# Performance work log

Hardware: AMD Instinct MI355X
Metric: run time of the kernel (lower is better)

Reference implementation:

```python
import jax, jax.numpy as jnp
import numpy as np

HEADS = 8
NEG_SLOPE = 0.2  # PyG GATConv default LeakyReLU slope


def _gat_layer(x, src, dst, W, a_src, a_dst, bias, heads, out_ch):
    """PyG-style GATConv (concat heads, self-loops already appended, eval mode).
    x: [N, F_in]; src/dst: [E_tot] int; W: [F_in, heads*out_ch];
    a_src/a_dst: [heads, out_ch]; bias: [heads*out_ch].
    """
    N = x.shape[0]
    h = (x @ W).reshape(N, heads, out_ch)                      # [N, H, C]
    # per-node attention logits (gathered per edge as scalars, not features)
    al_s = jnp.einsum('nhc,hc->nh', h, a_src)                  # [N, H]
    al_d = jnp.einsum('nhc,hc->nh', h, a_dst)                  # [N, H]
    e = jax.nn.leaky_relu(al_s[src] + al_d[dst], negative_slope=NEG_SLOPE)  # [E, H]
    # segment softmax over incoming edges of each target node (stable)
    e_max = jax.ops.segment_max(e, dst, num_segments=N)        # self-loops => no empty segments
    ex = jnp.exp(e - e_max[dst])
    denom = jax.ops.segment_sum(ex, dst, num_segments=N)
    alpha = ex / (denom[dst] + 1e-16)                          # [E, H]
    # gather source features, weight, scatter-add to targets
    out = jax.ops.segment_sum(h[src] * alpha[:, :, None], dst, num_segments=N)  # [N, H, C]
    return out.reshape(N, heads * out_ch) + bias


def setup_inputs() -> dict:
    key = jax.random.key(0)
    ks = jax.random.split(key, 16)
    N, E, F_IN, NUM_CLASSES = 50000, 1600000, 128, 16
    s = 0.1
    return {
        'x': jax.random.normal(ks[0], (N, F_IN), dtype=jnp.float32),
        'edge_index': jax.random.randint(ks[1], (2, E), 0, N, dtype=jnp.int64),
        # GAT layer 1: 128 -> 8 heads x 8
        'W1': jax.random.normal(ks[2], (F_IN, 64), dtype=jnp.float32) * s,
        'a1_src': jax.random.normal(ks[3], (8, 8), dtype=jnp.float32) * s,
        'a1_dst': jax.random.normal(ks[4], (8, 8), dtype=jnp.float32) * s,
        'b1': jnp.zeros((64,), dtype=jnp.float32),
        # GAT layer 2: 64 -> 8 heads x 4
        'W2': jax.random.normal(ks[5], (64, 32), dtype=jnp.float32) * s,
        'a2_src': jax.random.normal(ks[6], (8, 4), dtype=jnp.float32) * s,
        'a2_dst': jax.random.normal(ks[7], (8, 4), dtype=jnp.float32) * s,
        'b2': jnp.zeros((32,), dtype=jnp.float32),
        # torch MultiheadAttention(32, 8): packed in_proj [96,32], out_proj [32,32]
        'in_proj_w': jax.random.normal(ks[8], (96, 32), dtype=jnp.float32) * s,
        'in_proj_b': jnp.zeros((96,), dtype=jnp.float32),
        'out_proj_w': jax.random.normal(ks[9], (32, 32), dtype=jnp.float32) * s,
        'out_proj_b': jnp.zeros((32,), dtype=jnp.float32),
        # fc: 32 -> num_classes
        'fc_w': jax.random.normal(ks[10], (NUM_CLASSES, 32), dtype=jnp.float32) * s,
        'fc_b': jnp.zeros((NUM_CLASSES,), dtype=jnp.float32),
    }


def reference(x, edge_index, W1, a1_src, a1_dst, b1, W2, a2_src, a2_dst, b2,
              in_proj_w, in_proj_b, out_proj_w, out_proj_b, fc_w, fc_b):
    N = x.shape[0]
    loops = jnp.arange(N, dtype=edge_index.dtype)
    src = jnp.concatenate([edge_index[0], loops])  # PyG add_self_loops=True
    dst = jnp.concatenate([edge_index[1], loops])

    h = jax.nn.elu(_gat_layer(x, src, dst, W1, a1_src, a1_dst, b1, HEADS, 8))   # [N, 64]
    h = jax.nn.elu(_gat_layer(h, src, dst, W2, a2_src, a2_dst, b2, HEADS, 4))   # [N, 32]

    # MultiheadAttention on h.unsqueeze(0): shape [1, N, 32] with torch's
    # seq-first layout => seq_len = 1, batch = N. Softmax over a single key
    # is identically 1 for every head, so out = out_proj(v_proj(h)).
    v = h @ in_proj_w[64:96].T + in_proj_b[64:96]   # v-projection slice of packed in_proj
    h = v @ out_proj_w.T + out_proj_b               # [N, 32]

    logits = h @ fc_w.T + fc_b                      # [N, num_classes]
    return jax.nn.log_softmax(logits, axis=1)
```

## Files before the change

### kernel.cpp

```cpp
#include <hip/hip_runtime.h>
#include <hip/hip_bf16.h>
#include <math.h>


#define BSHIFT 7
#define BMASK  ((1 << BSHIFT) - 1)
#define MAXNB  512
#define TILE   8192
#define XST    136
#define SMBYTES 36864
#define LESRC_MAX 6144

typedef __attribute__((ext_vector_type(8))) short short8;
typedef __attribute__((ext_vector_type(4))) float floatx4;
typedef __attribute__((ext_vector_type(2))) float floatx2;

__device__ __forceinline__ unsigned short f2bf(float f) {
    union { float f; unsigned int u; } v; v.f = f;
    unsigned int u = v.u;
    return (unsigned short)((u + 0x7FFFu + ((u >> 16) & 1u)) >> 16);
}
__device__ __forceinline__ float lrelu(float e) { return fmaxf(e, 0.2f * e); }
__device__ __forceinline__ float elu(float o) {
    return (o > 0.f) ? o : (__expf(o) - 1.f);
}

__global__ __launch_bounds__(256) void fused_pre_kernel(
    const float* __restrict__ x, const float* __restrict__ W,
    const float* __restrict__ a_src, const float* __restrict__ a_dst,
    char* __restrict__ rec1, float* __restrict__ ald, int N, int GB,
    const int* __restrict__ ei, int E, int Et, int NB, int CAP,
    int* __restrict__ gcount, unsigned int* __restrict__ rec, int NT,
    const float* __restrict__ in_proj_w, const float* __restrict__ in_proj_b,
    const float* __restrict__ out_proj_w, const float* __restrict__ out_proj_b,
    const float* __restrict__ fc_w, const float* __restrict__ fc_b,
    float* __restrict__ M, float* __restrict__ bf) {
    __shared__ __align__(16) char sm[SMBYTES];
    int t = threadIdx.x;
    int bid = blockIdx.x;
    if (bid < GB) {
        unsigned short* xs = (unsigned short*)sm;
        unsigned short* wt = xs + 64 * XST;
        int nb = bid * 64;
// ... 2 lines not shown
            int p = t + 256 * r;
            int row = p >> 5;
            int c4  = p & 31;
            int n = nb + row;
            float4 v = (n < N) ? ((const float4*)x)[(size_t)n * 32 + c4]
                               : make_float4(0.f, 0.f, 0.f, 0.f);
            unsigned short* dst = &xs[row * XST + c4 * 4];
            dst[0] = f2bf(v.x); dst[1] = f2bf(v.y);
            dst[2] = f2bf(v.z); dst[3] = f2bf(v.w);
        }
        {
            int n = t & 63, kg = t >> 6;
#pragma unroll
            for (int c = 0; c < 4; ++c) {
                int k0 = kg * 32 + c * 8;
                unsigned short* dst = &wt[n * XST + k0];
#pragma unroll
                for (int j = 0; j < 8; ++j)
                    dst[j] = f2bf(W[(k0 + j) * 64 + n]);
            }
        }
        __syncthreads();
        int wave = t >> 6, lane = t & 63;
        int m16 = lane & 15, quad = lane >> 4;
        floatx4 acc[4];
#pragma unroll
        for (int i = 0; i < 4; ++i) acc[i] = (floatx4){0.f, 0.f, 0.f, 0.f};
#pragma unroll
        for (int k = 0; k < 4; ++k) {
            int koff = k * 32 + quad * 8;
            short8 afrag = *(const short8*)&xs[(wave * 16 + m16) * XST + koff];
#pragma unroll
            for (int nt = 0; nt < 4; ++nt) {
                short8 bfrag = *(const short8*)&wt[(nt * 16 + m16) * XST + koff];
// ... 5 lines not shown
#pragma unroll
        for (int nt = 0; nt < 4; ++nt)
#pragma unroll
            for (int r = 0; r < 4; ++r)
                hs[(wave * 16 + quad * 4 + r) * 65 + nt * 16 + m16] = acc[nt][r];
        __syncthreads();
        float asv = a_src[lane], adv = a_dst[lane];
        for (int itn = 0; itn < 16; ++itn) {
            int nl = wave * 16 + itn;
            int n = nb + nl;
            if (n >= N) break;
            float v = hs[nl * 65 + lane];
            float ps = v * asv, pd = v * adv;
            ps += __shfl_xor(ps, 1); ps += __shfl_xor(ps, 2); ps += __shfl_xor(ps, 4);
            pd += __shfl_xor(pd, 1); pd += __shfl_xor(pd, 2); pd += __shfl_xor(pd, 4);
            if ((lane & 7) == 0) {
                *(float*)(rec1 + (size_t)n * 128 + 4 * (lane >> 3)) = ps;
                ald[n * 8 + (lane >> 3)] = pd;
            }
            if (lane < 16) {
                const float* hr = &hs[nl * 65 + lane * 4];
                int pk = __builtin_amdgcn_cvt_pk_fp8_f32(hr[0], hr[1], 0, false);
                pk = __builtin_amdgcn_cvt_pk_fp8_f32(hr[2], hr[3], pk, true);
                *(unsigned*)(rec1 + (size_t)n * 128 + 64 + 4 * lane) = (unsigned)pk;
            }
        }
    } else if (bid < GB + NT) {
        unsigned int* lrec = (unsigned int*)sm;
        int* h   = (int*)(sm + TILE * 4);
        int* cur = (int*)(sm + TILE * 4 + MAXNB * 4);
        for (int i = t; i < NB; i += 256) h[i] = 0;
        int tile0 = (bid - GB) * TILE;
        int cnt = Et - tile0; if (cnt > TILE) cnt = TILE;
        __syncthreads();
        for (int j = t; j < cnt; j += 256) {
            int jj = tile0 + j;
            int srcv, d;
            if (jj < E) { srcv = ei[jj]; d = ei[E + jj]; } else { srcv = jj - E; d = jj - E; }
            lrec[j] = (unsigned)srcv | ((unsigned)d << 16);
// ... 89 lines not shown
    for (int i = t; i < cnt; i += 256)
        esrc[obase + i] = lesrc[i];
}

__global__ __launch_bounds__(256) void gat_agg64_g2_kernel(
    const int* __restrict__ rowp, const unsigned short* __restrict__ esrc,
    const char* __restrict__ rec1, const float* __restrict__ ald_arr,
    const float* __restrict__ bias,
    const float* __restrict__ W2, const float* __restrict__ a2s,
    const float* __restrict__ a2d,
    char* __restrict__ rec2, float* __restrict__ ald2, int N) {
    __shared__ __align__(16) float W2p[2][8][32][4];
    __shared__ __align__(16) float oL[4][64];
    __shared__ __align__(16) float h2L[4][32];
    int t = threadIdx.x;
    for (int idx = t; idx < 2048; idx += 256) {
        int k = idx >> 5, l = idx & 31;
        W2p[k >> 5][(k & 31) >> 2][l][k & 3] = W2[idx];
    }
    __syncthreads();
    const int lane = t & 63;
    const int wv = t >> 6;
    const int e = lane >> 3;
    const int c = lane & 7;
    const int aoff = 4 * c;
    const int foff = 64 + 8 * c;
    int n = blockIdx.x * 4 + wv;
    if (n >= N) return;
    float aldv = ald_arr[n * 8 + c];
    int beg = rowp[n], end = rowp[n + 1];
    float dA = 0.f, dB = 0.f;
    floatx2 A0 = {0.f, 0.f}, A1 = {0.f, 0.f}, A2 = {0.f, 0.f}, A3 = {0.f, 0.f};
    floatx2 B0 = {0.f, 0.f}, B1 = {0.f, 0.f}, B2 = {0.f, 0.f}, B3 = {0.f, 0.f};
    int i = beg;
    for (; i + 32 <= end; i += 32) {
        int s0 = esrc[i + e],      s1 = esrc[i + 8 + e];
        int s2 = esrc[i + 16 + e], s3 = esrc[i + 24 + e];
        const char* r0 = rec1 + (size_t)s0 * 128;
        const char* r1 = rec1 + (size_t)s1 * 128;
        const char* r2 = rec1 + (size_t)s2 * 128;
        const char* r3 = rec1 + (size_t)s3 * 128;
        float e0 = *(const float*)(r0 + aoff), e1 = *(const float*)(r1 + aoff);
        float e2 = *(const float*)(r2 + aoff), e3 = *(const float*)(r3 + aoff);
        uint2 g0 = *(const uint2*)(r0 + foff), g1 = *(const uint2*)(r1 + foff);
        uint2 g2 = *(const uint2*)(r2 + foff), g3 = *(const uint2*)(r3 + foff);
        float w0 = __expf(lrelu(e0 + aldv));
        float w1 = __expf(lrelu(e1 + aldv));
        float w2 = __expf(lrelu(e2 + aldv));
        float w3 = __expf(lrelu(e3 + aldv));
        dA += w0 + w2; dB += w1 + w3;
        A0 += w0 * __builtin_amdgcn_cvt_pk_f32_fp8(g0.x, false);
        A1 += w0 * __builtin_amdgcn_cvt_pk_f32_fp8(g0.x, true);
        A2 += w0 * __builtin_amdgcn_cvt_pk_f32_fp8(g0.y, false);
        A3 += w0 * __builtin_amdgcn_cvt_pk_f32_fp8(g0.y, true);
        B0 += w1 * __builtin_amdgcn_cvt_pk_f32_fp8(g1.x, false);
        B1 += w1 * __builtin_amdgcn_cvt_pk_f32_fp8(g1.x, true);
        B2 += w1 * __builtin_amdgcn_cvt_pk_f32_fp8(g1.y, false);
        B3 += w1 * __builtin_amdgcn_cvt_pk_f32_fp8(g1.y, true);
        A0 += w2 * __builtin_amdgcn_cvt_pk_f32_fp8(g2.x, false);
        A1 += w2 * __builtin_amdgcn_cvt_pk_f32_fp8(g2.x, true);
        A2 += w2 * __builtin_amdgcn_cvt_pk_f32_fp8(g2.y, false);
        A3 += w2 * __builtin_amdgcn_cvt_pk_f32_fp8(g2.y, true);
        B0 += w3 * __builtin_amdgcn_cvt_pk_f32_fp8(g3.x, false);
        B1 += w3 * __builtin_amdgcn_cvt_pk_f32_fp8(g3.x, true);
        B2 += w3 * __builtin_amdgcn_cvt_pk_f32_fp8(g3.y, false);
        B3 += w3 * __builtin_amdgcn_cvt_pk_f32_fp8(g3.y, true);
    }
    for (; i < end; i += 32) {
        int i0 = i + e, i1 = i + 8 + e, i2 = i + 16 + e, i3 = i + 24 + e;
        bool v0 = i0 < end, v1 = i1 < end, v2 = i2 < end, v3 = i3 < end;
        int c0 = v0 ? i0 : beg;
        int c1 = v1 ? i1 : beg;
        int c2 = v2 ? i2 : beg;
        int c3 = v3 ? i3 : beg;
        int s0 = esrc[c0], s1 = esrc[c1], s2 = esrc[c2], s3 = esrc[c3];
        const char* r0 = rec1 + (size_t)s0 * 128;
        const char* r1 = rec1 + (size_t)s1 * 128;
        const char* r2 = rec1 + (size_t)s2 * 128;
        const char* r3 = rec1 + (size_t)s3 * 128;
        float e0 = *(const float*)(r0 + aoff), e1 = *(const float*)(r1 + aoff);
        float e2 = *(const float*)(r2 + aoff), e3 = *(const float*)(r3 + aoff);
        uint2 g0 = *(const uint2*)(r0 + foff), g1 = *(const uint2*)(r1 + foff);
        uint2 g2 = *(const uint2*)(r2 + foff), g3 = *(const uint2*)(r3 + foff);
        float w0 = v0 ? __expf(lrelu(e0 + aldv)) : 0.f;
        float w1 = v1 ? __expf(lrelu(e1 + aldv)) : 0.f;
        float w2 = v2 ? __expf(lrelu(e2 + aldv)) : 0.f;
        float w3 = v3 ? __expf(lrelu(e3 + aldv)) : 0.f;
        dA += w0 + w2; dB += w1 + w3;
        A0 += w0 * __builtin_amdgcn_cvt_pk_f32_fp8(g0.x, false);
        A1 += w0 * __builtin_amdgcn_cvt_pk_f32_fp8(g0.x, true);
        A2 += w0 * __builtin_amdgcn_cvt_pk_f32_fp8(g0.y, false);
        A3 += w0 * __builtin_amdgcn_cvt_pk_f32_fp8(g0.y, true);
        B0 += w1 * __builtin_amdgcn_cvt_pk_f32_fp8(g1.x, false);
        B1 += w1 * __builtin_amdgcn_cvt_pk_f32_fp8(g1.x, true);
        B2 += w1 * __builtin_amdgcn_cvt_pk_f32_fp8(g1.y, false);
        B3 += w1 * __builtin_amdgcn_cvt_pk_f32_fp8(g1.y, true);
        A0 += w2 * __builtin_amdgcn_cvt_pk_f32_fp8(g2.x, false);
        A1 += w2 * __builtin_amdgcn_cvt_pk_f32_fp8(g2.x, true);
        A2 += w2 * __builtin_amdgcn_cvt_pk_f32_fp8(g2.y, false);
        A3 += w2 * __builtin_amdgcn_cvt_pk_f32_fp8(g2.y, true);
        B0 += w3 * __builtin_amdgcn_cvt_pk_f32_fp8(g3.x, false);
        B1 += w3 * __builtin_amdgcn_cvt_pk_f32_fp8(g3.x, true);
        B2 += w3 * __builtin_amdgcn_cvt_pk_f32_fp8(g3.y, false);
        B3 += w3 * __builtin_amdgcn_cvt_pk_f32_fp8(g3.y, true);
    }
    float d = dA + dB;
    float P0 = A0.x + B0.x, P1 = A0.y + B0.y;
    float P2 = A1.x + B1.x, P3 = A1.y + B1.y;
    float P4 = A2.x + B2.x, P5 = A2.y + B2.y;
    float P6 = A3.x + B3.x, P7 = A3.y + B3.y;
    d  += __shfl_xor(d, 8);  d  += __shfl_xor(d, 16);  d  += __shfl_xor(d, 32);
    P0 += __shfl_xor(P0, 8); P0 += __shfl_xor(P0, 16); P0 += __shfl_xor(P0, 32);
    P1 += __shfl_xor(P1, 8); P1 += __shfl_xor(P1, 16); P1 += __shfl_xor(P1, 32);
    P2 += __shfl_xor(P2, 8); P2 += __shfl_xor(P2, 16); P2 += __shfl_xor(P2, 32);
    P3 += __shfl_xor(P3, 8); P3 += __shfl_xor(P3, 16); P3 += __shfl_xor(P3, 32);
    P4 += __shfl_xor(P4, 8); P4 += __shfl_xor(P4, 16); P4 += __shfl_xor(P4, 32);
    P5 += __shfl_xor(P5, 8); P5 += __shfl_xor(P5, 16); P5 += __shfl_xor(P5, 32);
    P6 += __shfl_xor(P6, 8); P6 += __shfl_xor(P6, 16); P6 += __shfl_xor(P6, 32);
    P7 += __shfl_xor(P7, 8); P7 += __shfl_xor(P7, 16); P7 += __shfl_xor(P7, 32);
    float inv = 1.f / (d + 1e-16f);
    float4 bv0 = ((const float4*)bias)[2 * c];
    float4 bv1 = ((const float4*)bias)[2 * c + 1];
    float o0 = elu(P0 * inv + bv0.x);
    float o1 = elu(P1 * inv + bv0.y);
    float o2 = elu(P2 * inv + bv0.z);
    float o3 = elu(P3 * inv + bv0.w);
    float o4 = elu(P4 * inv + bv1.x);
    float o5 = elu(P5 * inv + bv1.y);
    float o6 = elu(P6 * inv + bv1.z);
    float o7 = elu(P7 * inv + bv1.w);
    if (lane < 8) {
        *(float4*)&oL[wv][c * 8]     = make_float4(o0, o1, o2, o3);
        *(float4*)&oL[wv][c * 8 + 4] = make_float4(o4, o5, o6, o7);
    }
    const int l = lane & 31, kh = lane >> 5;
    const float* orow = &oL[wv][kh * 32];
    float a0 = 0.f, a1 = 0.f, a2 = 0.f, a3 = 0.f;
#pragma unroll
    for (int g = 0; g < 8; ++g) {
        float4 ov = *(const float4*)&orow[g * 4];
        float4 wv4 = *(const float4*)&W2p[kh][g][l][0];
        a0 += ov.x * wv4.x; a1 += ov.y * wv4.y;
        a2 += ov.z * wv4.z; a3 += ov.w * wv4.w;
    }
    float acc = (a0 + a1) + (a2 + a3);
    acc += __shfl_xor(acc, 32);
    float ps = acc * a2s[l], pd = acc * a2d[l];
    ps += __shfl_xor(ps, 1); ps += __shfl_xor(ps, 2);
    pd += __shfl_xor(pd, 1); pd += __shfl_xor(pd, 2);
    if (lane < 32) {
        h2L[wv][l] = acc;
        if ((l & 3) == 0) {
            *(float*)(rec2 + (size_t)n * 64 + 4 * (l >> 2)) = ps;
            ald2[n * 8 + (l >> 2)] = pd;
        }
    }
    if (lane < 8) {
        const float* hr = &h2L[wv][lane * 4];
        int pk = __builtin_amdgcn_cvt_pk_fp8_f32(hr[0], hr[1], 0, false);
        pk = __builtin_amdgcn_cvt_pk_fp8_f32(hr[2], hr[3], pk, true);
        *(unsigned*)(rec2 + (size_t)n * 64 + 32 + 4 * lane) = (unsigned)pk;
    }
}

__global__ __launch_bounds__(256) void gat_agg32_fin_kernel(
    const int* __restrict__ rowp, const unsigned short* __restrict__ esrc,
    const char* __restrict__ rec2, const float* __restrict__ ald_arr,
    const float* __restrict__ bias,
    const float* __restrict__ M, const float* __restrict__ bf,
    float* __restrict__ out, int N) {
    __shared__ __align__(16) float Mp[8][16][4];
    __shared__ float bfs[16];
    __shared__ __align__(16) float oL[4][32];
    int t = threadIdx.x;
    for (int i = t; i < 512; i += 256) {
        int j = i >> 5, k = i & 31;
        Mp[k >> 2][j][k & 3] = M[i];
    }
    if (t < 16) bfs[t] = bf[t];
    __syncthreads();
    const int lane = t & 63;
    const int wv = t >> 6;
    const int e = lane >> 3;
    const int c = lane & 7;
    const int aoff = 4 * c;
    const int foff = 32 + 4 * c;
    int n = blockIdx.x * 4 + wv;
    if (n >= N) return;
    float aldv = ald_arr[n * 8 + c];
    int beg = rowp[n], end = rowp[n + 1];
    float d0 = 0.f, d1 = 0.f, d2 = 0.f, d3 = 0.f;
    floatx2 p0a = {0.f, 0.f}, p0b = {0.f, 0.f};
    floatx2 p1a = {0.f, 0.f}, p1b = {0.f, 0.f};
    floatx2 p2a = {0.f, 0.f}, p2b = {0.f, 0.f};
    floatx2 p3a = {0.f, 0.f}, p3b = {0.f, 0.f};
    int base = beg;
    for (; base + 32 <= end; base += 32) {
        int s0 = esrc[base + e],      s1 = esrc[base + 8 + e];
        int s2 = esrc[base + 16 + e], s3 = esrc[base + 24 + e];
        const char* r0 = rec2 + (size_t)s0 * 64;
        const char* r1 = rec2 + (size_t)s1 * 64;
        const char* r2 = rec2 + (size_t)s2 * 64;
        const char* r3 = rec2 + (size_t)s3 * 64;
        float e0 = *(const float*)(r0 + aoff) + aldv;
        float e1 = *(const float*)(r1 + aoff) + aldv;
        float e2 = *(const float*)(r2 + aoff) + aldv;
        float e3 = *(const float*)(r3 + aoff) + aldv;
        unsigned g0 = *(const unsigned*)(r0 + foff);
        unsigned g1 = *(const unsigned*)(r1 + foff);
        unsigned g2 = *(const unsigned*)(r2 + foff);
        unsigned g3 = *(const unsigned*)(r3 + foff);
        float w0 = __expf(lrelu(e0));
        float w1 = __expf(lrelu(e1));
        float w2 = __expf(lrelu(e2));
        float w3 = __expf(lrelu(e3));
        d0 += w0; d1 += w1; d2 += w2; d3 += w3;
        p0a += w0 * __builtin_amdgcn_cvt_pk_f32_fp8(g0, false);
        p0b += w0 * __builtin_amdgcn_cvt_pk_f32_fp8(g0, true);
        p1a += w1 * __builtin_amdgcn_cvt_pk_f32_fp8(g1, false);
        p1b += w1 * __builtin_amdgcn_cvt_pk_f32_fp8(g1, true);
        p2a += w2 * __builtin_amdgcn_cvt_pk_f32_fp8(g2, false);
        p2b += w2 * __builtin_amdgcn_cvt_pk_f32_fp8(g2, true);
        p3a += w3 * __builtin_amdgcn_cvt_pk_f32_fp8(g3, false);
        p3b += w3 * __builtin_amdgcn_cvt_pk_f32_fp8(g3, true);
    }
    for (; base < end; base += 32) {
        int i0 = base + e;
        int i1 = base + 8 + e;
        int i2 = base + 16 + e;
        int i3 = base + 24 + e;
        bool v0 = i0 < end, v1 = i1 < end, v2 = i2 < end, v3 = i3 < end;
        int c0 = v0 ? i0 : beg;
        int c1 = v1 ? i1 : beg;
        int c2 = v2 ? i2 : beg;
        int c3 = v3 ? i3 : beg;
        int s0 = esrc[c0], s1 = esrc[c1], s2 = esrc[c2], s3 = esrc[c3];
        const char* r0 = rec2 + (size_t)s0 * 64;
        const char* r1 = rec2 + (size_t)s1 * 64;
        const char* r2 = rec2 + (size_t)s2 * 64;
        const char* r3 = rec2 + (size_t)s3 * 64;
        float e0 = *(const float*)(r0 + aoff) + aldv;
        float e1 = *(const float*)(r1 + aoff) + aldv;
        float e2 = *(const float*)(r2 + aoff) + aldv;
        float e3 = *(const float*)(r3 + aoff) + aldv;
        unsigned g0 = *(const unsigned*)(r0 + foff);
        unsigned g1 = *(const unsigned*)(r1 + foff);
        unsigned g2 = *(const unsigned*)(r2 + foff);
        unsigned g3 = *(const unsigned*)(r3 + foff);
        float w0 = v0 ? __expf(lrelu(e0)) : 0.f;
        float w1 = v1 ? __expf(lrelu(e1)) : 0.f;
        float w2 = v2 ? __expf(lrelu(e2)) : 0.f;
        float w3 = v3 ? __expf(lrelu(e3)) : 0.f;
        d0 += w0; d1 += w1; d2 += w2; d3 += w3;
        p0a += w0 * __builtin_amdgcn_cvt_pk_f32_fp8(g0, false);
        p0b += w0 * __builtin_amdgcn_cvt_pk_f32_fp8(g0, true);
        p1a += w1 * __builtin_amdgcn_cvt_pk_f32_fp8(g1, false);
        p1b += w1 * __builtin_amdgcn_cvt_pk_f32_fp8(g1, true);
        p2a += w2 * __builtin_amdgcn_cvt_pk_f32_fp8(g2, false);
        p2b += w2 * __builtin_amdgcn_cvt_pk_f32_fp8(g2, true);
        p3a += w3 * __builtin_amdgcn_cvt_pk_f32_fp8(g3, false);
        p3b += w3 * __builtin_amdgcn_cvt_pk_f32_fp8(g3, true);
    }
    float d = (d0 + d1) + (d2 + d3);
    floatx2 Pa = (p0a + p1a) + (p2a + p3a);
    floatx2 Pb = (p0b + p1b) + (p2b + p3b);
    float P0 = Pa.x, P1 = Pa.y, P2 = Pb.x, P3 = Pb.y;
    d  += __shfl_xor(d, 8);  d  += __shfl_xor(d, 16);  d  += __shfl_xor(d, 32);
    P0 += __shfl_xor(P0, 8); P0 += __shfl_xor(P0, 16); P0 += __shfl_xor(P0, 32);
    P1 += __shfl_xor(P1, 8); P1 += __shfl_xor(P1, 16); P1 += __shfl_xor(P1, 32);
    P2 += __shfl_xor(P2, 8); P2 += __shfl_xor(P2, 16); P2 += __shfl_xor(P2, 32);
    P3 += __shfl_xor(P3, 8); P3 += __shfl_xor(P3, 16); P3 += __shfl_xor(P3, 32);
    float inv = 1.f / (d + 1e-16f);
    float4 bv = ((const float4*)bias)[c];
    float o0 = elu(P0 * inv + bv.x);
    float o1 = elu(P1 * inv + bv.y);
    float o2 = elu(P2 * inv + bv.z);
    float o3 = elu(P3 * inv + bv.w);
    if (lane < 8) *(float4*)&oL[wv][c * 4] = make_float4(o0, o1, o2, o3);
    const int j = lane & 15;
    const float* orow = oL[wv];
    float a0 = 0.f, a1 = 0.f, a2 = 0.f, a3 = 0.f;
#pragma unroll
    for (int g = 0; g < 8; ++g) {
        float4 ov = *(const float4*)&orow[g * 4];
        float4 mv = *(const float4*)&Mp[g][j][0];
        a0 += ov.x * mv.x; a1 += ov.y * mv.y;
        a2 += ov.z * mv.z; a3 += ov.w * mv.w;
    }
    float logit = (a0 + a1) + (a2 + a3) + bfs[j];
    float mx = logit;
    mx = fmaxf(mx, __shfl_xor(mx, 1));
    mx = fmaxf(mx, __shfl_xor(mx, 2));
    mx = fmaxf(mx, __shfl_xor(mx, 4));
// ... 46 lines not shown
        void* p = ws + off;
        off += bytes;
        off = (off + 255) & ~(size_t)255;
        return p;
    };
    int*   bcount = (int*)alloc(MAXNB * 4);
    unsigned int*   rec  = (unsigned int*)alloc((size_t)NB * CAP * 4);
    int*   rowp   = (int*)alloc((size_t)(N + 1) * 4);
    unsigned short* esrc = (unsigned short*)alloc((size_t)Et * 2);
    char* rec1   = (char*)alloc((size_t)N * 128);
    float* al1d  = (float*)alloc((size_t)N * 8 * 4);
    char* rec2   = (char*)alloc((size_t)N * 64);
    float* al2d  = (float*)alloc((size_t)N * 8 * 4);
    float* Mf    = (float*)alloc(512 * 4);
    float* bff   = (float*)alloc(16 * 4);
    (void)ws_size; (void)n_in; (void)out_size;

    hipMemsetAsync(bcount, 0, MAXNB * 4, stream);
    fused_pre_kernel<<<GB + NTILES + 1, 256, 0, stream>>>(
        x, W1, a1s, a1d, rec1, al1d, N, GB,
        ei, E, Et, NB, CAP, bcount, rec, NTILES,
        ipw, ipb, opw, opb, fcw, fcb, Mf, bff);
    csr_finalize_kernel<<<NB, 256, 0, stream>>>(rec, bcount, rowp, esrc, N, Et, CAP);

    gat_agg64_g2_kernel<<<(N + 3) / 4, 256, 0, stream>>>(
        rowp, esrc, rec1, al1d, b1, W2, a2s, a2d, rec2, al2d, N);
    gat_agg32_fin_kernel<<<(N + 3) / 4, 256, 0, stream>>>(
        rowp, esrc, rec2, al2d, b2, Mf, bff, out, N);
}
```

Baseline: 212.3 us.

## Interleave per-head logits with fp8 features and fully unroll low-degree gathers

The layer-1 node record is changed so each head stores its attention logit next to its 8 fp8 features in one 16-byte chunk. The aggregation kernel can then fetch both with a single uint4 load per edge instead of separate float and uint2 loads. Both aggregation kernels add a fast path for nodes with degree up to 48 or 64 that issues all gathers up front, which gives more memory-level parallelism. The W2/M shared-memory staging moves after the gather so it overlaps with the loads. A small prep kernel also pre-converts W1 to bf16 and replaces the memset, at the cost of an extra launch and padded record bytes.

```diff
diff --git a/kernel.cpp b/kernel.cpp
--- a/kernel.cpp
+++ b/kernel.cpp
@@ -25,8 +25,18 @@
     return (o > 0.f) ? o : (__expf(o) - 1.f);
 }
 
+__global__ __launch_bounds__(256) void prep_kernel(
+    const float* __restrict__ W, unsigned short* __restrict__ wtb,
+    int* __restrict__ gcount) {
+    int t = threadIdx.x;
+    if (blockIdx.x == 0) { gcount[t] = 0; gcount[t + 256] = 0; }
+    int idx = blockIdx.x * 256 + t;
+    int n = idx >> 7, k = idx & 127;
+    wtb[idx] = f2bf(W[k * 64 + n]);
+}
+
 __global__ __launch_bounds__(256) void fused_pre_kernel(
-    const float* __restrict__ x, const float* __restrict__ W,
+    const float* __restrict__ x, const unsigned short* __restrict__ wtb,
     const float* __restrict__ a_src, const float* __restrict__ a_dst,
     char* __restrict__ rec1, float* __restrict__ ald, int N, int GB,
     const int* __restrict__ ei, int E, int Et, int NB, int CAP,
@@ -59,10 +69,7 @@
 #pragma unroll
             for (int c = 0; c < 4; ++c) {
                 int k0 = kg * 32 + c * 8;
-                unsigned short* dst = &wt[n * XST + k0];
-#pragma unroll
-                for (int j = 0; j < 8; ++j)
-                    dst[j] = f2bf(W[(k0 + j) * 64 + n]);
+                *(short8*)&wt[n * XST + k0] = *(const short8*)&wtb[n * 128 + k0];
             }
         }
         __syncthreads();
@@ -98,15 +105,21 @@
             float ps = v * asv, pd = v * adv;
             ps += __shfl_xor(ps, 1); ps += __shfl_xor(ps, 2); ps += __shfl_xor(ps, 4);
             pd += __shfl_xor(pd, 1); pd += __shfl_xor(pd, 2); pd += __shfl_xor(pd, 4);
-            if ((lane & 7) == 0) {
-                *(float*)(rec1 + (size_t)n * 128 + 4 * (lane >> 3)) = ps;
+            float av = __shfl(ps, (lane & 7) * 8);
+            if ((lane & 7) == 0)
                 ald[n * 8 + (lane >> 3)] = pd;
-            }
-            if (lane < 16) {
-                const float* hr = &hs[nl * 65 + lane * 4];
-                int pk = __builtin_amdgcn_cvt_pk_fp8_f32(hr[0], hr[1], 0, false);
-                pk = __builtin_amdgcn_cvt_pk_fp8_f32(hr[2], hr[3], pk, true);
-                *(unsigned*)(rec1 + (size_t)n * 128 + 64 + 4 * lane) = (unsigned)pk;
+            if (lane < 8) {
+                const float* hr = &hs[nl * 65 + lane * 8];
+                int pk0 = __builtin_amdgcn_cvt_pk_fp8_f32(hr[0], hr[1], 0, false);
+                pk0 = __builtin_amdgcn_cvt_pk_fp8_f32(hr[2], hr[3], pk0, true);
+                int pk1 = __builtin_amdgcn_cvt_pk_fp8_f32(hr[4], hr[5], 0, false);
+                pk1 = __builtin_amdgcn_cvt_pk_fp8_f32(hr[6], hr[7], pk1, true);
+                uint4 w4;
+                w4.x = __float_as_uint(av);
+                w4.y = (unsigned)pk0;
+                w4.z = (unsigned)pk1;
+                w4.w = 0u;
+                *(uint4*)(rec1 + (size_t)n * 128 + lane * 16) = w4;
             }
         }
     } else if (bid < GB + NT) {
@@ -226,125 +239,150 @@
     __shared__ __align__(16) float oL[4][64];
     __shared__ __align__(16) float h2L[4][32];
     int t = threadIdx.x;
-    for (int idx = t; idx < 2048; idx += 256) {
-        int k = idx >> 5, l = idx & 31;
-        W2p[k >> 5][(k & 31) >> 2][l][k & 3] = W2[idx];
-    }
-    __syncthreads();
     const int lane = t & 63;
     const int wv = t >> 6;
     const int e = lane >> 3;
     const int c = lane & 7;
-    const int aoff = 4 * c;
-    const int foff = 64 + 8 * c;
     int n = blockIdx.x * 4 + wv;
-    if (n >= N) return;
-    float aldv = ald_arr[n * 8 + c];
-    int beg = rowp[n], end = rowp[n + 1];
-    float dA = 0.f, dB = 0.f;
-    floatx2 A0 = {0.f, 0.f}, A1 = {0.f, 0.f}, A2 = {0.f, 0.f}, A3 = {0.f, 0.f};
-    floatx2 B0 = {0.f, 0.f}, B1 = {0.f, 0.f}, B2 = {0.f, 0.f}, B3 = {0.f, 0.f};
-    int i = beg;
-    for (; i + 32 <= end; i += 32) {
-        int s0 = esrc[i + e],      s1 = esrc[i + 8 + e];
-        int s2 = esrc[i + 16 + e], s3 = esrc[i + 24 + e];
-        const char* r0 = rec1 + (size_t)s0 * 128;
-        const char* r1 = rec1 + (size_t)s1 * 128;
-        const char* r2 = rec1 + (size_t)s2 * 128;
-        const char* r3 = rec1 + (size_t)s3 * 128;
-        float e0 = *(const float*)(r0 + aoff), e1 = *(const float*)(r1 + aoff);
-        float e2 = *(const float*)(r2 + aoff), e3 = *(const float*)(r3 + aoff);
-        uint2 g0 = *(const uint2*)(r0 + foff), g1 = *(const uint2*)(r1 + foff);
-        uint2 g2 = *(const uint2*)(r2 + foff), g3 = *(const uint2*)(r3 + foff);
-        float w0 = __expf(lrelu(e0 + aldv));
-        float w1 = __expf(lrelu(e1 + aldv));
-        float w2 = __expf(lrelu(e2 + aldv));
-        float w3 = __expf(lrelu(e3 + aldv));
-        dA += w0 + w2; dB += w1 + w3;
-        A0 += w0 * __builtin_amdgcn_cvt_pk_f32_fp8(g0.x, false);
-        A1 += w0 * __builtin_amdgcn_cvt_pk_f32_fp8(g0.x, true);
-        A2 += w0 * __builtin_amdgcn_cvt_pk_f32_fp8(g0.y, false);
-        A3 += w0 * __builtin_amdgcn_cvt_pk_f32_fp8(g0.y, true);
-        B0 += w1 * __builtin_amdgcn_cvt_pk_f32_fp8(g1.x, false);
-        B1 += w1 * __builtin_amdgcn_cvt_pk_f32_fp8(g1.x, true);
-        B2 += w1 * __builtin_amdgcn_cvt_pk_f32_fp8(g1.y, false);
-        B3 += w1 * __builtin_amdgcn_cvt_pk_f32_fp8(g1.y, true);
-        A0 += w2 * __builtin_amdgcn_cvt_pk_f32_fp8(g2.x, false);
-        A1 += w2 * __builtin_amdgcn_cvt_pk_f32_fp8(g2.x, true);
-        A2 += w2 * __builtin_amdgcn_cvt_pk_f32_fp8(g2.y, false);
-        A3 += w2 * __builtin_amdgcn_cvt_pk_f32_fp8(g2.y, true);
-        B0 += w3 * __builtin_amdgcn_cvt_pk_f32_fp8(g3.x, false);
-        B1 += w3 * __builtin_amdgcn_cvt_pk_f32_fp8(g3.x, true);
-        B2 += w3 * __builtin_amdgcn_cvt_pk_f32_fp8(g3.y, false);
-        B3 += w3 * __builtin_amdgcn_cvt_pk_f32_fp8(g3.y, true);
-    }
-    for (; i < end; i += 32) {
-        int i0 = i + e, i1 = i + 8 + e, i2 = i + 16 + e, i3 = i + 24 + e;
-        bool v0 = i0 < end, v1 = i1 < end, v2 = i2 < end, v3 = i3 < end;
-        int c0 = v0 ? i0 : beg;
-        int c1 = v1 ? i1 : beg;
-        int c2 = v2 ? i2 : beg;
-        int c3 = v3 ? i3 : beg;
-        int s0 = esrc[c0], s1 = esrc[c1], s2 = esrc[c2], s3 = esrc[c3];
-        const char* r0 = rec1 + (size_t)s0 * 128;
-        const char* r1 = rec1 + (size_t)s1 * 128;
-        const char* r2 = rec1 + (size_t)s2 * 128;
-        const char* r3 = rec1 + (size_t)s3 * 128;
-        float e0 = *(const float*)(r0 + aoff), e1 = *(const float*)(r1 + aoff);
-        float e2 = *(const float*)(r2 + aoff), e3 = *(const float*)(r3 + aoff);
-        uint2 g0 = *(const uint2*)(r0 + foff), g1 = *(const uint2*)(r1 + foff);
-        uint2 g2 = *(const uint2*)(r2 + foff), g3 = *(const uint2*)(r3 + foff);
-        float w0 = v0 ? __expf(lrelu(e0 + aldv)) : 0.f;
-        float w1 = v1 ? __expf(lrelu(e1 + aldv)) : 0.f;
-        float w2 = v2 ? __expf(lrelu(e2 + aldv)) : 0.f;
-        float w3 = v3 ? __expf(lrelu(e3 + aldv)) : 0.f;
-        dA += w0 + w2; dB += w1 + w3;
-        A0 += w0 * __builtin_amdgcn_cvt_pk_f32_fp8(g0.x, false);
-        A1 += w0 * __builtin_amdgcn_cvt_pk_f32_fp8(g0.x, true);
-        A2 += w0 * __builtin_amdgcn_cvt_pk_f32_fp8(g0.y, false);
-        A3 += w0 * __builtin_amdgcn_cvt_pk_f32_fp8(g0.y, true);
-        B0 += w1 * __builtin_amdgcn_cvt_pk_f32_fp8(g1.x, false);
-        B1 += w1 * __builtin_amdgcn_cvt_pk_f32_fp8(g1.x, true);
-        B2 += w1 * __builtin_amdgcn_cvt_pk_f32_fp8(g1.y, false);
-        B3 += w1 * __builtin_amdgcn_cvt_pk_f32_fp8(g1.y, true);
-        A0 += w2 * __builtin_amdgcn_cvt_pk_f32_fp8(g2.x, false);
-        A1 += w2 * __builtin_amdgcn_cvt_pk_f32_fp8(g2.x, true);
-        A2 += w2 * __builtin_amdgcn_cvt_pk_f32_fp8(g2.y, false);
-        A3 += w2 * __builtin_amdgcn_cvt_pk_f32_fp8(g2.y, true);
-        B0 += w3 * __builtin_amdgcn_cvt_pk_f32_fp8(g3.x, false);
-        B1 += w3 * __builtin_amdgcn_cvt_pk_f32_fp8(g3.x, true);
-        B2 += w3 * __builtin_amdgcn_cvt_pk_f32_fp8(g3.y, false);
-        B3 += w3 * __builtin_amdgcn_cvt_pk_f32_fp8(g3.y, true);
-    }
-    float d = dA + dB;
-    float P0 = A0.x + B0.x, P1 = A0.y + B0.y;
-    float P2 = A1.x + B1.x, P3 = A1.y + B1.y;
-    float P4 = A2.x + B2.x, P5 = A2.y + B2.y;
-    float P6 = A3.x + B3.x, P7 = A3.y + B3.y;
-    d  += __shfl_xor(d, 8);  d  += __shfl_xor(d, 16);  d  += __shfl_xor(d, 32);
-    P0 += __shfl_xor(P0, 8); P0 += __shfl_xor(P0, 16); P0 += __shfl_xor(P0, 32);
-    P1 += __shfl_xor(P1, 8); P1 += __shfl_xor(P1, 16); P1 += __shfl_xor(P1, 32);
-    P2 += __shfl_xor(P2, 8); P2 += __shfl_xor(P2, 16); P2 += __shfl_xor(P2, 32);
-    P3 += __shfl_xor(P3, 8); P3 += __shfl_xor(P3, 16); P3 += __shfl_xor(P3, 32);
-    P4 += __shfl_xor(P4, 8); P4 += __shfl_xor(P4, 16); P4 += __shfl_xor(P4, 32);
-    P5 += __shfl_xor(P5, 8); P5 += __shfl_xor(P5, 16); P5 += __shfl_xor(P5, 32);
-    P6 += __shfl_xor(P6, 8); P6 += __shfl_xor(P6, 16); P6 += __shfl_xor(P6, 32);
-    P7 += __shfl_xor(P7, 8); P7 += __shfl_xor(P7, 16); P7 += __shfl_xor(P7, 32);
-    float inv = 1.f / (d + 1e-16f);
-    float4 bv0 = ((const float4*)bias)[2 * c];
-    float4 bv1 = ((const float4*)bias)[2 * c + 1];
-    float o0 = elu(P0 * inv + bv0.x);
-    float o1 = elu(P1 * inv + bv0.y);
-    float o2 = elu(P2 * inv + bv0.z);
-    float o3 = elu(P3 * inv + bv0.w);
-    float o4 = elu(P4 * inv + bv1.x);
-    float o5 = elu(P5 * inv + bv1.y);
-    float o6 = elu(P6 * inv + bv1.z);
-    float o7 = elu(P7 * inv + bv1.w);
-    if (lane < 8) {
-        *(float4*)&oL[wv][c * 8]     = make_float4(o0, o1, o2, o3);
-        *(float4*)&oL[wv][c * 8 + 4] = make_float4(o4, o5, o6, o7);
-    }
+    bool active = n < N;
+    if (active) {
+        float aldv = ald_arr[n * 8 + c];
+        int beg = rowp[n], end = rowp[n + 1];
+        int deg = end - beg;
+        float dA = 0.f, dB = 0.f;
+        floatx2 A0 = {0.f, 0.f}, A1 = {0.f, 0.f}, A2 = {0.f, 0.f}, A3 = {0.f, 0.f};
+        floatx2 B0 = {0.f, 0.f}, B1 = {0.f, 0.f}, B2 = {0.f, 0.f}, B3 = {0.f, 0.f};
+        if (deg <= 48) {
+            int s[6];
+#pragma unroll
+            for (int g = 0; g < 6; ++g) {
+                int p = beg + g * 8 + e;
+                s[g] = esrc[(p < end) ? p : beg];
+            }
+            uint4 r[6];
+#pragma unroll
+            for (int g = 0; g < 6; ++g)
+                r[g] = *(const uint4*)(rec1 + (size_t)s[g] * 128 + c * 16);
+#pragma unroll
+            for (int g = 0; g < 6; ++g) {
+                bool vv = (beg + g * 8 + e) < end;
+                float w = vv ? __expf(lrelu(__uint_as_float(r[g].x) + aldv)) : 0.f;
+                if ((g & 1) == 0) {
+                    dA += w;
+                    A0 += w * __builtin_amdgcn_cvt_pk_f32_fp8(r[g].y, false);
+                    A1 += w * __builtin_amdgcn_cvt_pk_f32_fp8(r[g].y, true);
+                    A2 += w * __builtin_amdgcn_cvt_pk_f32_fp8(r[g].z, false);
+                    A3 += w * __builtin_amdgcn_cvt_pk_f32_fp8(r[g].z, true);
+                } else {
+                    dB += w;
+                    B0 += w * __builtin_amdgcn_cvt_pk_f32_fp8(r[g].y, false);
+                    B1 += w * __builtin_amdgcn_cvt_pk_f32_fp8(r[g].y, true);
+                    B2 += w * __builtin_amdgcn_cvt_pk_f32_fp8(r[g].z, false);
+                    B3 += w * __builtin_amdgcn_cvt_pk_f32_fp8(r[g].z, true);
+                }
+            }
+        } else {
+            int i = beg;
+            for (; i + 32 <= end; i += 32) {
+                int s0 = esrc[i + e],      s1 = esrc[i + 8 + e];
+                int s2 = esrc[i + 16 + e], s3 = esrc[i + 24 + e];
+                uint4 r0 = *(const uint4*)(rec1 + (size_t)s0 * 128 + c * 16);
+                uint4 r1 = *(const uint4*)(rec1 + (size_t)s1 * 128 + c * 16);
+                uint4 r2 = *(const uint4*)(rec1 + (size_t)s2 * 128 + c * 16);
+                uint4 r3 = *(const uint4*)(rec1 + (size_t)s3 * 128 + c * 16);
+                float w0 = __expf(lrelu(__uint_as_float(r0.x) + aldv));
+                float w1 = __expf(lrelu(__uint_as_float(r1.x) + aldv));
+                float w2 = __expf(lrelu(__uint_as_float(r2.x) + aldv));
+                float w3 = __expf(lrelu(__uint_as_float(r3.x) + aldv));
+                dA += w0 + w2; dB += w1 + w3;
+                A0 += w0 * __builtin_amdgcn_cvt_pk_f32_fp8(r0.y, false);
+                A1 += w0 * __builtin_amdgcn_cvt_pk_f32_fp8(r0.y, true);
+                A2 += w0 * __builtin_amdgcn_cvt_pk_f32_fp8(r0.z, false);
+                A3 += w0 * __builtin_amdgcn_cvt_pk_f32_fp8(r0.z, true);
+                B0 += w1 * __builtin_amdgcn_cvt_pk_f32_fp8(r1.y, false);
+                B1 += w1 * __builtin_amdgcn_cvt_pk_f32_fp8(r1.y, true);
+                B2 += w1 * __builtin_amdgcn_cvt_pk_f32_fp8(r1.z, false);
+                B3 += w1 * __builtin_amdgcn_cvt_pk_f32_fp8(r1.z, true);
+                A0 += w2 * __builtin_amdgcn_cvt_pk_f32_fp8(r2.y, false);
+                A1 += w2 * __builtin_amdgcn_cvt_pk_f32_fp8(r2.y, true);
+                A2 += w2 * __builtin_amdgcn_cvt_pk_f32_fp8(r2.z, false);
+                A3 += w2 * __builtin_amdgcn_cvt_pk_f32_fp8(r2.z, true);
+                B0 += w3 * __builtin_amdgcn_cvt_pk_f32_fp8(r3.y, false);
+                B1 += w3 * __builtin_amdgcn_cvt_pk_f32_fp8(r3.y, true);
+                B2 += w3 * __builtin_amdgcn_cvt_pk_f32_fp8(r3.z, false);
+                B3 += w3 * __builtin_amdgcn_cvt_pk_f32_fp8(r3.z, true);
+            }
+            for (; i < end; i += 32) {
+                int i0 = i + e, i1 = i + 8 + e, i2 = i + 16 + e, i3 = i + 24 + e;
+                bool v0 = i0 < end, v1 = i1 < end, v2 = i2 < end, v3 = i3 < end;
+                int c0 = v0 ? i0 : beg;
+                int c1 = v1 ? i1 : beg;
+                int c2 = v2 ? i2 : beg;
+                int c3 = v3 ? i3 : beg;
+                int s0 = esrc[c0], s1 = esrc[c1], s2 = esrc[c2], s3 = esrc[c3];
+                uint4 r0 = *(const uint4*)(rec1 + (size_t)s0 * 128 + c * 16);
+                uint4 r1 = *(const uint4*)(rec1 + (size_t)s1 * 128 + c * 16);
+                uint4 r2 = *(const uint4*)(rec1 + (size_t)s2 * 128 + c * 16);
+                uint4 r3 = *(const uint4*)(rec1 + (size_t)s3 * 128 + c * 16);
+                float w0 = v0 ? __expf(lrelu(__uint_as_float(r0.x) + aldv)) : 0.f;
+                float w1 = v1 ? __expf(lrelu(__uint_as_float(r1.x) + aldv)) : 0.f;
+                float w2 = v2 ? __expf(lrelu(__uint_as_float(r2.x) + aldv)) : 0.f;
+                float w3 = v3 ? __expf(lrelu(__uint_as_float(r3.x) + aldv)) : 0.f;
+                dA += w0 + w2; dB += w1 + w3;
+                A0 += w0 * __builtin_amdgcn_cvt_pk_f32_fp8(r0.y, false);
+                A1 += w0 * __builtin_amdgcn_cvt_pk_f32_fp8(r0.y, true);
+                A2 += w0 * __builtin_amdgcn_cvt_pk_f32_fp8(r0.z, false);
+                A3 += w0 * __builtin_amdgcn_cvt_pk_f32_fp8(r0.z, true);
+                B0 += w1 * __builtin_amdgcn_cvt_pk_f32_fp8(r1.y, false);
+                B1 += w1 * __builtin_amdgcn_cvt_pk_f32_fp8(r1.y, true);
+                B2 += w1 * __builtin_amdgcn_cvt_pk_f32_fp8(r1.z, false);
+                B3 += w1 * __builtin_amdgcn_cvt_pk_f32_fp8(r1.z, true);
+                A0 += w2 * __builtin_amdgcn_cvt_pk_f32_fp8(r2.y, false);
+                A1 += w2 * __builtin_amdgcn_cvt_pk_f32_fp8(r2.y, true);
+                A2 += w2 * __builtin_amdgcn_cvt_pk_f32_fp8(r2.z, false);
+                A3 += w2 * __builtin_amdgcn_cvt_pk_f32_fp8(r2.z, true);
+                B0 += w3 * __builtin_amdgcn_cvt_pk_f32_fp8(r3.y, false);
+                B1 += w3 * __builtin_amdgcn_cvt_pk_f32_fp8(r3.y, true);
+                B2 += w3 * __builtin_amdgcn_cvt_pk_f32_fp8(r3.z, false);
+                B3 += w3 * __builtin_amdgcn_cvt_pk_f32_fp8(r3.z, true);
+            }
+        }
+        float d = dA + dB;
+        float P0 = A0.x + B0.x, P1 = A0.y + B0.y;
+        float P2 = A1.x + B1.x, P3 = A1.y + B1.y;
+        float P4 = A2.x + B2.x, P5 = A2.y + B2.y;
+        float P6 = A3.x + B3.x, P7 = A3.y + B3.y;
+        d  += __shfl_xor(d, 8);  d  += __shfl_xor(d, 16);  d  += __shfl_xor(d, 32);
+        P0 += __shfl_xor(P0, 8); P0 += __shfl_xor(P0, 16); P0 += __shfl_xor(P0, 32);
+        P1 += __shfl_xor(P1, 8); P1 += __shfl_xor(P1, 16); P1 += __shfl_xor(P1, 32);
+        P2 += __shfl_xor(P2, 8); P2 += __shfl_xor(P2, 16); P2 += __shfl_xor(P2, 32);
+        P3 += __shfl_xor(P3, 8); P3 += __shfl_xor(P3, 16); P3 += __shfl_xor(P3, 32);
+        P4 += __shfl_xor(P4, 8); P4 += __shfl_xor(P4, 16); P4 += __shfl_xor(P4, 32);
+        P5 += __shfl_xor(P5, 8); P5 += __shfl_xor(P5, 16); P5 += __shfl_xor(P5, 32);
+        P6 += __shfl_xor(P6, 8); P6 += __shfl_xor(P6, 16); P6 += __shfl_xor(P6, 32);
+        P7 += __shfl_xor(P7, 8); P7 += __shfl_xor(P7, 16); P7 += __shfl_xor(P7, 32);
+        float inv = 1.f / (d + 1e-16f);
+        float4 bv0 = ((const float4*)bias)[2 * c];
+        float4 bv1 = ((const float4*)bias)[2 * c + 1];
+        float o0 = elu(P0 * inv + bv0.x);
+        float o1 = elu(P1 * inv + bv0.y);
+        float o2 = elu(P2 * inv + bv0.z);
+        float o3 = elu(P3 * inv + bv0.w);
+        float o4 = elu(P4 * inv + bv1.x);
+        float o5 = elu(P5 * inv + bv1.y);
+        float o6 = elu(P6 * inv + bv1.z);
+        float o7 = elu(P7 * inv + bv1.w);
+        if (lane < 8) {
+            *(float4*)&oL[wv][c * 8]     = make_float4(o0, o1, o2, o3);
+            *(float4*)&oL[wv][c * 8 + 4] = make_float4(o4, o5, o6, o7);
+        }
+    }
+    for (int idx = t; idx < 2048; idx += 256) {
+        int k = idx >> 5, l = idx & 31;
+        W2p[k >> 5][(k & 31) >> 2][l][k & 3] = W2[idx];
+    }
+    __syncthreads();
+    if (!active) return;
     const int l = lane & 31, kh = lane >> 5;
     const float* orow = &oL[wv][kh * 32];
     float a0 = 0.f, a1 = 0.f, a2 = 0.f, a3 = 0.f;
@@ -360,18 +398,19 @@
     float ps = acc * a2s[l], pd = acc * a2d[l];
     ps += __shfl_xor(ps, 1); ps += __shfl_xor(ps, 2);
     pd += __shfl_xor(pd, 1); pd += __shfl_xor(pd, 2);
+    float psv = __shfl(ps, (lane & 7) * 4);
     if (lane < 32) {
         h2L[wv][l] = acc;
-        if ((l & 3) == 0) {
-            *(float*)(rec2 + (size_t)n * 64 + 4 * (l >> 2)) = ps;
-            ald2[n * 8 + (l >> 2)] = pd;
-        }
+        if ((l & 3) == 0) ald2[n * 8 + (l >> 2)] = pd;
     }
     if (lane < 8) {
         const float* hr = &h2L[wv][lane * 4];
         int pk = __builtin_amdgcn_cvt_pk_fp8_f32(hr[0], hr[1], 0, false);
         pk = __builtin_amdgcn_cvt_pk_fp8_f32(hr[2], hr[3], pk, true);
-        *(unsigned*)(rec2 + (size_t)n * 64 + 32 + 4 * lane) = (unsigned)pk;
+        uint2 w2;
+        w2.x = __float_as_uint(psv);
+        w2.y = (unsigned)pk;
+        *(uint2*)(rec2 + (size_t)n * 64 + lane * 8) = w2;
     }
 }
 
@@ -385,110 +424,131 @@
     __shared__ float bfs[16];
     __shared__ __align__(16) float oL[4][32];
     int t = threadIdx.x;
-    for (int i = t; i < 512; i += 256) {
-        int j = i >> 5, k = i & 31;
-        Mp[k >> 2][j][k & 3] = M[i];
-    }
-    if (t < 16) bfs[t] = bf[t];
-    __syncthreads();
     const int lane = t & 63;
     const int wv = t >> 6;
     const int e = lane >> 3;
     const int c = lane & 7;
-    const int aoff = 4 * c;
-    const int foff = 32 + 4 * c;
     int n = blockIdx.x * 4 + wv;
-    if (n >= N) return;
-    float aldv = ald_arr[n * 8 + c];
-    int beg = rowp[n], end = rowp[n + 1];
-    float d0 = 0.f, d1 = 0.f, d2 = 0.f, d3 = 0.f;
-    floatx2 p0a = {0.f, 0.f}, p0b = {0.f, 0.f};
-    floatx2 p1a = {0.f, 0.f}, p1b = {0.f, 0.f};
-    floatx2 p2a = {0.f, 0.f}, p2b = {0.f, 0.f};
-    floatx2 p3a = {0.f, 0.f}, p3b = {0.f, 0.f};
-    int base = beg;
-    for (; base + 32 <= end; base += 32) {
-        int s0 = esrc[base + e],      s1 = esrc[base + 8 + e];
-        int s2 = esrc[base + 16 + e], s3 = esrc[base + 24 + e];
-        const char* r0 = rec2 + (size_t)s0 * 64;
-        const char* r1 = rec2 + (size_t)s1 * 64;
-        const char* r2 = rec2 + (size_t)s2 * 64;
-        const char* r3 = rec2 + (size_t)s3 * 64;
-        float e0 = *(const float*)(r0 + aoff) + aldv;
-        float e1 = *(const float*)(r1 + aoff) + aldv;
-        float e2 = *(const float*)(r2 + aoff) + aldv;
-        float e3 = *(const float*)(r3 + aoff) + aldv;
-        unsigned g0 = *(const unsigned*)(r0 + foff);
-        unsigned g1 = *(const unsigned*)(r1 + foff);
-        unsigned g2 = *(const unsigned*)(r2 + foff);
-        unsigned g3 = *(const unsigned*)(r3 + foff);
-        float w0 = __expf(lrelu(e0));
-        float w1 = __expf(lrelu(e1));
-        float w2 = __expf(lrelu(e2));
-        float w3 = __expf(lrelu(e3));
-        d0 += w0; d1 += w1; d2 += w2; d3 += w3;
-        p0a += w0 * __builtin_amdgcn_cvt_pk_f32_fp8(g0, false);
-        p0b += w0 * __builtin_amdgcn_cvt_pk_f32_fp8(g0, true);
-        p1a += w1 * __builtin_amdgcn_cvt_pk_f32_fp8(g1, false);
-        p1b += w1 * __builtin_amdgcn_cvt_pk_f32_fp8(g1, true);
-        p2a += w2 * __builtin_amdgcn_cvt_pk_f32_fp8(g2, false);
-        p2b += w2 * __builtin_amdgcn_cvt_pk_f32_fp8(g2, true);
-        p3a += w3 * __builtin_amdgcn_cvt_pk_f32_fp8(g3, false);
-        p3b += w3 * __builtin_amdgcn_cvt_pk_f32_fp8(g3, true);
-    }
-    for (; base < end; base += 32) {
-        int i0 = base + e;
-        int i1 = base + 8 + e;
-        int i2 = base + 16 + e;
-        int i3 = base + 24 + e;
-        bool v0 = i0 < end, v1 = i1 < end, v2 = i2 < end, v3 = i3 < end;
-        int c0 = v0 ? i0 : beg;
-        int c1 = v1 ? i1 : beg;
-        int c2 = v2 ? i2 : beg;
-        int c3 = v3 ? i3 : beg;
-        int s0 = esrc[c0], s1 = esrc[c1], s2 = esrc[c2], s3 = esrc[c3];
-        const char* r0 = rec2 + (size_t)s0 * 64;
-        const char* r1 = rec2 + (size_t)s1 * 64;
-        const char* r2 = rec2 + (size_t)s2 * 64;
-        const char* r3 = rec2 + (size_t)s3 * 64;
-        float e0 = *(const float*)(r0 + aoff) + aldv;
-        float e1 = *(const float*)(r1 + aoff) + aldv;
-        float e2 = *(const float*)(r2 + aoff) + aldv;
-        float e3 = *(const float*)(r3 + aoff) + aldv;
-        unsigned g0 = *(const unsigned*)(r0 + foff);
-        unsigned g1 = *(const unsigned*)(r1 + foff);
-        unsigned g2 = *(const unsigned*)(r2 + foff);
-        unsigned g3 = *(const unsigned*)(r3 + foff);
-        float w0 = v0 ? __expf(lrelu(e0)) : 0.f;
-        float w1 = v1 ? __expf(lrelu(e1)) : 0.f;
-        float w2 = v2 ? __expf(lrelu(e2)) : 0.f;
-        float w3 = v3 ? __expf(lrelu(e3)) : 0.f;
-        d0 += w0; d1 += w1; d2 += w2; d3 += w3;
-        p0a += w0 * __builtin_amdgcn_cvt_pk_f32_fp8(g0, false);
-        p0b += w0 * __builtin_amdgcn_cvt_pk_f32_fp8(g0, true);
-        p1a += w1 * __builtin_amdgcn_cvt_pk_f32_fp8(g1, false);
-        p1b += w1 * __builtin_amdgcn_cvt_pk_f32_fp8(g1, true);
-        p2a += w2 * __builtin_amdgcn_cvt_pk_f32_fp8(g2, false);
-        p2b += w2 * __builtin_amdgcn_cvt_pk_f32_fp8(g2, true);
-        p3a += w3 * __builtin_amdgcn_cvt_pk_f32_fp8(g3, false);
-        p3b += w3 * __builtin_amdgcn_cvt_pk_f32_fp8(g3, true);
-    }
-    float d = (d0 + d1) + (d2 + d3);
-    floatx2 Pa = (p0a + p1a) + (p2a + p3a);
-    floatx2 Pb = (p0b + p1b) + (p2b + p3b);
-    float P0 = Pa.x, P1 = Pa.y, P2 = Pb.x, P3 = Pb.y;
-    d  += __shfl_xor(d, 8);  d  += __shfl_xor(d, 16);  d  += __shfl_xor(d, 32);
-    P0 += __shfl_xor(P0, 8); P0 += __shfl_xor(P0, 16); P0 += __shfl_xor(P0, 32);
-    P1 += __shfl_xor(P1, 8); P1 += __shfl_xor(P1, 16); P1 += __shfl_xor(P1, 32);
-    P2 += __shfl_xor(P2, 8); P2 += __shfl_xor(P2, 16); P2 += __shfl_xor(P2, 32);
-    P3 += __shfl_xor(P3, 8); P3 += __shfl_xor(P3, 16); P3 += __shfl_xor(P3, 32);
-    float inv = 1.f / (d + 1e-16f);
-    float4 bv = ((const float4*)bias)[c];
-    float o0 = elu(P0 * inv + bv.x);
-    float o1 = elu(P1 * inv + bv.y);
-    float o2 = elu(P2 * inv + bv.z);
-    float o3 = elu(P3 * inv + bv.w);
-    if (lane < 8) *(float4*)&oL[wv][c * 4] = make_float4(o0, o1, o2, o3);
+    bool active = n < N;
+    if (active) {
+        float aldv = ald_arr[n * 8 + c];
+        int beg = rowp[n], end = rowp[n + 1];
+        int deg = end - beg;
+        float d0 = 0.f, d1 = 0.f, d2 = 0.f, d3 = 0.f;
+        floatx2 p0a = {0.f, 0.f}, p0b = {0.f, 0.f};
+        floatx2 p1a = {0.f, 0.f}, p1b = {0.f, 0.f};
+        floatx2 p2a = {0.f, 0.f}, p2b = {0.f, 0.f};
+        floatx2 p3a = {0.f, 0.f}, p3b = {0.f, 0.f};
+        if (deg <= 64) {
+            int s[8];
+#pragma unroll
+            for (int g = 0; g < 8; ++g) {
+                int p = beg + g * 8 + e;
+                s[g] = esrc[(p < end) ? p : beg];
+            }
+            uint2 rr[8];
+#pragma unroll
+            for (int g = 0; g < 8; ++g)
+                rr[g] = *(const uint2*)(rec2 + (size_t)s[g] * 64 + c * 8);
+#pragma unroll
+            for (int g = 0; g < 8; ++g) {
+                bool vv = (beg + g * 8 + e) < end;
+                float w = vv ? __expf(lrelu(__uint_as_float(rr[g].x) + aldv)) : 0.f;
+                if ((g & 3) == 0) {
+                    d0 += w;
+                    p0a += w * __builtin_amdgcn_cvt_pk_f32_fp8(rr[g].y, false);
+                    p0b += w * __builtin_amdgcn_cvt_pk_f32_fp8(rr[g].y, true);
+                } else if ((g & 3) == 1) {
+                    d1 += w;
+                    p1a += w * __builtin_amdgcn_cvt_pk_f32_fp8(rr[g].y, false);
+                    p1b += w * __builtin_amdgcn_cvt_pk_f32_fp8(rr[g].y, true);
+                } else if ((g & 3) == 2) {
+                    d2 += w;
+                    p2a += w * __builtin_amdgcn_cvt_pk_f32_fp8(rr[g].y, false);
+                    p2b += w * __builtin_amdgcn_cvt_pk_f32_fp8(rr[g].y, true);
+                } else {
+                    d3 += w;
+                    p3a += w * __builtin_amdgcn_cvt_pk_f32_fp8(rr[g].y, false);
+                    p3b += w * __builtin_amdgcn_cvt_pk_f32_fp8(rr[g].y, true);
+                }
+            }
+        } else {
+            int base = beg;
+            for (; base + 32 <= end; base += 32) {
+                int s0 = esrc[base + e],      s1 = esrc[base + 8 + e];
+                int s2 = esrc[base + 16 + e], s3 = esrc[base + 24 + e];
+                uint2 r0 = *(const uint2*)(rec2 + (size_t)s0 * 64 + c * 8);
+                uint2 r1 = *(const uint2*)(rec2 + (size_t)s1 * 64 + c * 8);
+                uint2 r2 = *(const uint2*)(rec2 + (size_t)s2 * 64 + c * 8);
+                uint2 r3 = *(const uint2*)(rec2 + (size_t)s3 * 64 + c * 8);
+                float w0 = __expf(lrelu(__uint_as_float(r0.x) + aldv));
+                float w1 = __expf(lrelu(__uint_as_float(r1.x) + aldv));
+                float w2 = __expf(lrelu(__uint_as_float(r2.x) + aldv));
+                float w3 = __expf(lrelu(__uint_as_float(r3.x) + aldv));
+                d0 += w0; d1 += w1; d2 += w2; d3 += w3;
+                p0a += w0 * __builtin_amdgcn_cvt_pk_f32_fp8(r0.y, false);
+                p0b += w0 * __builtin_amdgcn_cvt_pk_f32_fp8(r0.y, true);
+                p1a += w1 * __builtin_amdgcn_cvt_pk_f32_fp8(r1.y, false);
+                p1b += w1 * __builtin_amdgcn_cvt_pk_f32_fp8(r1.y, true);
+                p2a += w2 * __builtin_amdgcn_cvt_pk_f32_fp8(r2.y, false);
+                p2b += w2 * __builtin_amdgcn_cvt_pk_f32_fp8(r2.y, true);
+                p3a += w3 * __builtin_amdgcn_cvt_pk_f32_fp8(r3.y, false);
+                p3b += w3 * __builtin_amdgcn_cvt_pk_f32_fp8(r3.y, true);
+            }
+            for (; base < end; base += 32) {
+                int i0 = base + e;
+                int i1 = base + 8 + e;
+                int i2 = base + 16 + e;
+                int i3 = base + 24 + e;
+                bool v0 = i0 < end, v1 = i1 < end, v2 = i2 < end, v3 = i3 < end;
+                int c0 = v0 ? i0 : beg;
+                int c1 = v1 ? i1 : beg;
+                int c2 = v2 ? i2 : beg;
+                int c3 = v3 ? i3 : beg;
+                int s0 = esrc[c0], s1 = esrc[c1], s2 = esrc[c2], s3 = esrc[c3];
+                uint2 r0 = *(const uint2*)(rec2 + (size_t)s0 * 64 + c * 8);
+                uint2 r1 = *(const uint2*)(rec2 + (size_t)s1 * 64 + c * 8);
+                uint2 r2 = *(const uint2*)(rec2 + (size_t)s2 * 64 + c * 8);
+                uint2 r3 = *(const uint2*)(rec2 + (size_t)s3 * 64 + c * 8);
+                float w0 = v0 ? __expf(lrelu(__uint_as_float(r0.x) + aldv)) : 0.f;
+                float w1 = v1 ? __expf(lrelu(__uint_as_float(r1.x) + aldv)) : 0.f;
+                float w2 = v2 ? __expf(lrelu(__uint_as_float(r2.x) + aldv)) : 0.f;
+                float w3 = v3 ? __expf(lrelu(__uint_as_float(r3.x) + aldv)) : 0.f;
+                d0 += w0; d1 += w1; d2 += w2; d3 += w3;
+                p0a += w0 * __builtin_amdgcn_cvt_pk_f32_fp8(r0.y, false);
+                p0b += w0 * __builtin_amdgcn_cvt_pk_f32_fp8(r0.y, true);
+                p1a += w1 * __builtin_amdgcn_cvt_pk_f32_fp8(r1.y, false);
+                p1b += w1 * __builtin_amdgcn_cvt_pk_f32_fp8(r1.y, true);
+                p2a += w2 * __builtin_amdgcn_cvt_pk_f32_fp8(r2.y, false);
+                p2b += w2 * __builtin_amdgcn_cvt_pk_f32_fp8(r2.y, true);
+                p3a += w3 * __builtin_amdgcn_cvt_pk_f32_fp8(r3.y, false);
+                p3b += w3 * __builtin_amdgcn_cvt_pk_f32_fp8(r3.y, true);
+            }
+        }
+        float d = (d0 + d1) + (d2 + d3);
+        floatx2 Pa = (p0a + p1a) + (p2a + p3a);
+        floatx2 Pb = (p0b + p1b) + (p2b + p3b);
+        float P0 = Pa.x, P1 = Pa.y, P2 = Pb.x, P3 = Pb.y;
+        d  += __shfl_xor(d, 8);  d  += __shfl_xor(d, 16);  d  += __shfl_xor(d, 32);
+        P0 += __shfl_xor(P0, 8); P0 += __shfl_xor(P0, 16); P0 += __shfl_xor(P0, 32);
+        P1 += __shfl_xor(P1, 8); P1 += __shfl_xor(P1, 16); P1 += __shfl_xor(P1, 32);
+        P2 += __shfl_xor(P2, 8); P2 += __shfl_xor(P2, 16); P2 += __shfl_xor(P2, 32);
+        P3 += __shfl_xor(P3, 8); P3 += __shfl_xor(P3, 16); P3 += __shfl_xor(P3, 32);
+        float inv = 1.f / (d + 1e-16f);
+        float4 bv = ((const float4*)bias)[c];
+        float o0 = elu(P0 * inv + bv.x);
+        float o1 = elu(P1 * inv + bv.y);
+        float o2 = elu(P2 * inv + bv.z);
+        float o3 = elu(P3 * inv + bv.w);
+        if (lane < 8) *(float4*)&oL[wv][c * 4] = make_float4(o0, o1, o2, o3);
+    }
+    for (int i = t; i < 512; i += 256) {
+        int j = i >> 5, k = i & 31;
+        Mp[k >> 2][j][k & 3] = M[i];
+    }
+    if (t < 16) bfs[t] = bf[t];
+    __syncthreads();
+    if (!active) return;
     const int j = lane & 15;
     const float* orow = oL[wv];
     float a0 = 0.f, a1 = 0.f, a2 = 0.f, a3 = 0.f;
@@ -565,11 +625,12 @@
     float* al2d  = (float*)alloc((size_t)N * 8 * 4);
     float* Mf    = (float*)alloc(512 * 4);
     float* bff   = (float*)alloc(16 * 4);
+    unsigned short* wtb = (unsigned short*)alloc(64 * 128 * 2);
     (void)ws_size; (void)n_in; (void)out_size;
 
-    hipMemsetAsync(bcount, 0, MAXNB * 4, stream);
+    prep_kernel<<<32, 256, 0, stream>>>(W1, wtb, bcount);
     fused_pre_kernel<<<GB + NTILES + 1, 256, 0, stream>>>(
-        x, W1, a1s, a1d, rec1, al1d, N, GB,
+        x, wtb, a1s, a1d, rec1, al1d, N, GB,
         ei, E, Et, NB, CAP, bcount, rec, NTILES,
         ipw, ipb, opw, opb, fcw, fcb, Mf, bff);
     csr_finalize_kernel<<<NB, 256, 0, stream>>>(rec, bcount, rowp, esrc, N, Et, CAP);
```

Result: no change. 208.5 us (-1.8%).
